# Kernel tuning notes

Measured on AMD Instinct MI355X. Metric: run time of the kernel, lower is better.

The kernel has to match this reference:

```python
import jax, jax.numpy as jnp
import numpy as np

NEUMANN_TERMS = 6  # matches neumann_terms=6 in init_kwargs


def cayley_apply(W, x, terms):
    """Apply Cayley-parameterized unitary U = (I - A)^{-1}(I + A), A = skew(W),
    with the inverse approximated by a truncated Neumann series:
    (I - A)^{-1} z ~= sum_{k=0}^{terms-1} A^k z.  x: [N, d] row vectors."""
    A = 0.5 * (W - W.T)            # skew-symmetric [d, d]
    z = x + x @ A.T                # (I + A) x
    acc = z
    s = z
    for _ in range(terms - 1):     # small fixed loop over Neumann terms
        s = s @ A.T                # A^k z
        acc = acc + s
    return acc


def quantum_activation(h, theta):
    """Parametric quantum rotation: rotate each adjacent feature pair by theta.
    Norm-preserving (unitary) nonlinearity in place of ReLU/GELU."""
    a = h[..., 0::2]
    b = h[..., 1::2]
    c = jnp.cos(theta)
    s = jnp.sin(theta)
    ra = a * c - b * s
    rb = a * s + b * c
    return jnp.stack([ra, rb], axis=-1).reshape(h.shape)


def setup_inputs() -> dict:
    key = jax.random.key(0)
    k1, k2, k3 = jax.random.split(key, 3)
    num_tokens, d_model = 16384, 2048
    x = jax.random.normal(k1, (num_tokens, d_model), dtype=jnp.float32)
    # Orthogonal(gain=0.1)-like init: small-norm weights keep the Neumann series convergent
    u1 = 0.1 * jax.random.normal(k2, (d_model, d_model), dtype=jnp.float32) / jnp.sqrt(d_model)
    u1 = u1 * jnp.sqrt(d_model) * 0.0 + 0.1 * jax.random.orthogonal(k2, d_model, dtype=jnp.float32)
    u2 = 0.1 * jax.random.orthogonal(k3, d_model, dtype=jnp.float32)
    theta = jnp.asarray(0.7854, dtype=jnp.float32)  # pi/4 initializer
    return {"x": x, "u1": u1, "u2": u2, "theta": theta}


def reference(x, u1, u2, theta):
    h = cayley_apply(u1, x, NEUMANN_TERMS)
    h = quantum_activation(h, theta)
    out = cayley_apply(u2, h, NEUMANN_TERMS)
    return out
```

## Files before the change

kernel.cpp:

```cpp
#include <hip/hip_runtime.h>
#include <hip/hip_bf16.h>

#define ND 2048

using bf16 = __hip_bfloat16;
using short8 = __attribute__((ext_vector_type(8))) short;
using floatx4 = __attribute__((ext_vector_type(4))) float;

__device__ __forceinline__ void gl2lds16(const short* g, short* l) {
    __builtin_amdgcn_global_load_lds(
        (const __attribute__((address_space(1))) unsigned int*)g,
        (__attribute__((address_space(3))) unsigned int*)l,
        16, 0, 0);
}


__global__ void build_skew(const float* __restrict__ u, bf16* __restrict__ M) {
    __shared__ float t[32][33];
    const int bx = blockIdx.x & (ND / 32 - 1);
    const int by = blockIdx.x / (ND / 32);
    const int tx = threadIdx.x & 31;
    const int ty = threadIdx.x >> 5;
#pragma unroll
    for (int rr = 0; rr < 4; ++rr) {
        const int r = ty * 4 + rr;
        t[tx][r] = u[(size_t)(bx * 32 + r) * ND + by * 32 + tx];
    }
    __syncthreads();
#pragma unroll
    for (int rr = 0; rr < 4; ++rr) {
        const int r = ty * 4 + rr;
        const size_t idx = (size_t)(by * 32 + r) * ND + bx * 32 + tx;
        M[idx] = __float2bfloat16(0.5f * (t[r][tx] - u[idx]));
    }
}

__global__ void build_hoff1(const bf16* __restrict__ M, const bf16* Msq, bf16* Hoff) {
    const size_t idx = (size_t)blockIdx.x * 256 + threadIdx.x;
    const float m = __bfloat162float(M[idx]);
    const float q = __bfloat162float(Msq[idx]);
    Hoff[idx] = __float2bfloat16(2.f * m + q);
}

__global__ void build_hoff(const bf16* M, const bf16* Msq, bf16* Hoff, bf16* HoffT) {
    const size_t idx = (size_t)blockIdx.x * 256 + threadIdx.x;
    const float m = __bfloat162float(M[idx]);
    const float q = __bfloat162float(Msq[idx]);
    Hoff[idx] = __float2bfloat16(2.f * m + q);
    HoffT[idx] = __float2bfloat16(q - 2.f * m);
}

__global__ void convert_f32_bf16(const float* __restrict__ x, bf16* __restrict__ y) {
    const size_t base = ((size_t)blockIdx.x * 256 + threadIdx.x) * 8;
    const float4 f0 = *(const float4*)(x + base);
    const float4 f1 = *(const float4*)(x + base + 4);
    short8 pk;
    pk[0] = __builtin_bit_cast(short, __float2bfloat16(f0.x));
    pk[1] = __builtin_bit_cast(short, __float2bfloat16(f0.y));
    pk[2] = __builtin_bit_cast(short, __float2bfloat16(f0.z));
    pk[3] = __builtin_bit_cast(short, __float2bfloat16(f0.w));
    pk[4] = __builtin_bit_cast(short, __float2bfloat16(f1.x));
    pk[5] = __builtin_bit_cast(short, __float2bfloat16(f1.y));
    pk[6] = __builtin_bit_cast(short, __float2bfloat16(f1.z));
    pk[7] = __builtin_bit_cast(short, __float2bfloat16(f1.w));
    *(short8*)((short*)y + base) = pk;
}

enum { EPI_PLAIN = 0, EPI_NEG = 1, EPI_ADD1 = 2, EPI_P = 3, EPI_P_ROT = 4, EPI_PT = 5 };

template <int EPI, bool OF32>
__device__ __forceinline__ void gemm_core(
    short* aT, short* bT,
    const bf16* __restrict__ A, const bf16* __restrict__ Bt, void* __restrict__ Cp,
    const int Nc, const int K, const int bx, const int by,
    const bf16* __restrict__ add1, const bf16* __restrict__ add2,
    const float* __restrict__ thetaP)
{
    const int tid = threadIdx.x;
    const int lane = tid & 63;
    const int quad = lane >> 4;
    const int l15 = lane & 15;
    const int wv = tid >> 6;
    const int wr = (wv >> 1) << 6;
    const int wc = (wv & 1) << 6;

    const short* Ag = (const short*)A + (size_t)(by << 7) * K;
    const short* Bg = (const short*)Bt + (size_t)(bx << 7) * K;

    floatx4 acc[4][4];
#pragma unroll
    for (int i = 0; i < 4; ++i)
#pragma unroll
        for (int j = 0; j < 4; ++j)
            acc[i][j] = (floatx4){0.f, 0.f, 0.f, 0.f};

    for (int k0 = 0; k0 < K; k0 += 32) {
#pragma unroll
        for (int c = 0; c < 2; ++c) {
            const int ch = (c << 8) + (wv << 6) + lane;
            const int row = ch >> 2;
            const int kp = (ch & 3) << 3;
            const int ldsBase = ((c << 8) + (wv << 6)) << 3;
            gl2lds16(Ag + (size_t)row * K + k0 + kp, aT + ldsBase);
            gl2lds16(Bg + (size_t)row * K + k0 + kp, bT + ldsBase);
        }
        __syncthreads();
        short8 af[4], bfr[4];
#pragma unroll
        for (int mi = 0; mi < 4; ++mi)
            af[mi] = *(const short8*)(aT + ((wr + (mi << 4) + l15) << 5) + (quad << 3));
#pragma unroll
        for (int ni = 0; ni < 4; ++ni)
            bfr[ni] = *(const short8*)(bT + ((wc + (ni << 4) + l15) << 5) + (quad << 3));
#pragma unroll
        for (int mi = 0; mi < 4; ++mi)
#pragma unroll
            for (int ni = 0; ni < 4; ++ni)
                acc[mi][ni] = __builtin_amdgcn_mfma_f32_16x16x32_bf16(af[mi], bfr[ni], acc[mi][ni], 0, 0, 0);
        __syncthreads();
    }

    float ct = 0.f, st = 0.f;
    if (EPI == EPI_P_ROT) {
        const float th = *thetaP;
        ct = cosf(th);
        st = sinf(th);
    }

#pragma unroll
    for (int mi = 0; mi < 4; ++mi) {
#pragma unroll
        for (int ni = 0; ni < 4; ++ni) {
#pragma unroll
            for (int r = 0; r < 4; ++r) {
                const int row = (by << 7) + wr + (mi << 4) + (quad << 2) + r;
                const int col = (bx << 7) + wc + (ni << 4) + l15;
                const size_t idx = (size_t)row * Nc + col;
                float v = acc[mi][ni][r];
                if (EPI == EPI_NEG) v = -v;
                if (EPI == EPI_ADD1) v += __bfloat162float(add1[idx]);
                if (EPI == EPI_P)
                    v += (row == col ? 1.f : 0.f)
                       + __bfloat162float(add1[idx]) + __bfloat162float(add2[idx]);
                if (EPI == EPI_PT)
                    v += (row == col ? 1.f : 0.f)
                       + __bfloat162float(add1[idx])
                       + __bfloat162float(add2[(size_t)col * Nc + row]);
                if (EPI == EPI_P_ROT) {
                    v += (row == col ? 1.f : 0.f)
                       + __bfloat162float(add1[idx]) + __bfloat162float(add2[idx]);
                    const float w = __shfl_xor(v, 1, 64);
                    v = (l15 & 1) ? (st * w + ct * v) : (ct * v - st * w);
                }
                if (OF32) ((float*)Cp)[idx] = v;
                else      ((bf16*)Cp)[idx] = __float2bfloat16(v);
            }
        }
    }
}

template <int EPI, bool OF32>
__launch_bounds__(256, 2) __global__
void gemm_one(const bf16* __restrict__ A, const bf16* __restrict__ Bt,
              void* __restrict__ Cp, const int Nc, const int K,
              const bf16* __restrict__ add1, const bf16* __restrict__ add2,
              const float* __restrict__ thetaP)
{
    __shared__ __attribute__((aligned(16))) short aT[128 * 32];
    __shared__ __attribute__((aligned(16))) short bT[128 * 32];
    const int nblk = Nc >> 7;
    gemm_core<EPI, OF32>(aT, bT, A, Bt, Cp, Nc, K, blockIdx.x % nblk, blockIdx.x / nblk,
                         add1, add2, thetaP);
}

template <int EPI0, int EPI1>
__launch_bounds__(256, 2) __global__
void gemm_dual(const bf16* A0, const bf16* B0, bf16* C0, const bf16* a10, const bf16* a20,
               const bf16* A1, const bf16* B1, bf16* C1, const bf16* a11, const bf16* a21,
               const float* thetaP)
{
    __shared__ __attribute__((aligned(16))) short aT[128 * 32];
    __shared__ __attribute__((aligned(16))) short bT[128 * 32];
    const int nblk = ND >> 7;
    const int nsub = nblk * nblk;
    int b = blockIdx.x;
    if (b < nsub) {
        gemm_core<EPI0, false>(aT, bT, A0, B0, (void*)C0, ND, ND, b % nblk, b / nblk, a10, a20, thetaP);
    } else {
        b -= nsub;
        gemm_core<EPI1, false>(aT, bT, A1, B1, (void*)C1, ND, ND, b % nblk, b / nblk, a11, a21, thetaP);
    }
}

template <int EPI, bool AF32, bool OF32>
__launch_bounds__(256, 2) __global__
void gemm_bt(const void* __restrict__ Ap, const bf16* __restrict__ Bt,
             void* __restrict__ Cp, const int Nc, const int K,
             const bf16* __restrict__ add1, const bf16* __restrict__ add2,
             const float* __restrict__ thetaP)
{
    __shared__ __attribute__((aligned(16))) short aT[128 * 32];
    __shared__ __attribute__((aligned(16))) short bT[128 * 32];

    const int nblk = Nc >> 7;
    const int bx = blockIdx.x % nblk;
    const int by = blockIdx.x / nblk;
    const int tid = threadIdx.x;
    const int lane = tid & 63;
    const int quad = lane >> 4;
    const int l15 = lane & 15;
    const int wv = tid >> 6;
    const int wr = (wv >> 1) << 6;
    const int wc = (wv & 1) << 6;

    const short* Ag = (const short*)Ap + (size_t)(by << 7) * K;
    const float* Agf = (const float*)Ap + (size_t)(by << 7) * K;
    const short* Bg = (const short*)Bt + (size_t)(bx << 7) * K;

    floatx4 acc[4][4];
#pragma unroll
    for (int i = 0; i < 4; ++i)
#pragma unroll
        for (int j = 0; j < 4; ++j)
            acc[i][j] = (floatx4){0.f, 0.f, 0.f, 0.f};

    for (int k0 = 0; k0 < K; k0 += 32) {
#pragma unroll
        for (int c = 0; c < 2; ++c) {
            const int ch = tid + (c << 8);
            const int row = ch >> 2;
            const int kp = (ch & 3) << 3;
            if (AF32) {
                const float4 f0 = *(const float4*)(Agf + (size_t)row * K + k0 + kp);
                const float4 f1 = *(const float4*)(Agf + (size_t)row * K + k0 + kp + 4);
                short8 pk;
                pk[0] = __builtin_bit_cast(short, __float2bfloat16(f0.x));
                pk[1] = __builtin_bit_cast(short, __float2bfloat16(f0.y));
                pk[2] = __builtin_bit_cast(short, __float2bfloat16(f0.z));
                pk[3] = __builtin_bit_cast(short, __float2bfloat16(f0.w));
                pk[4] = __builtin_bit_cast(short, __float2bfloat16(f1.x));
                pk[5] = __builtin_bit_cast(short, __float2bfloat16(f1.y));
                pk[6] = __builtin_bit_cast(short, __float2bfloat16(f1.z));
                pk[7] = __builtin_bit_cast(short, __float2bfloat16(f1.w));
                *(short8*)(aT + (row << 5) + kp) = pk;
            } else {
                *(int4*)(aT + (row << 5) + kp) = *(const int4*)(Ag + (size_t)row * K + k0 + kp);
            }
            *(int4*)(bT + (row << 5) + kp) = *(const int4*)(Bg + (size_t)row * K + k0 + kp);
        }
        __syncthreads();
        short8 af[4], bfr[4];
#pragma unroll
        for (int mi = 0; mi < 4; ++mi)
            af[mi] = *(const short8*)(aT + ((wr + (mi << 4) + l15) << 5) + (quad << 3));
#pragma unroll
        for (int ni = 0; ni < 4; ++ni)
            bfr[ni] = *(const short8*)(bT + ((wc + (ni << 4) + l15) << 5) + (quad << 3));
#pragma unroll
        for (int mi = 0; mi < 4; ++mi)
#pragma unroll
            for (int ni = 0; ni < 4; ++ni)
                acc[mi][ni] = __builtin_amdgcn_mfma_f32_16x16x32_bf16(af[mi], bfr[ni], acc[mi][ni], 0, 0, 0);
        __syncthreads();
    }

    float ct = 0.f, st = 0.f;
    if (EPI == EPI_P_ROT) {
        const float th = *thetaP;
        ct = cosf(th);
        st = sinf(th);
    }

#pragma unroll
    for (int mi = 0; mi < 4; ++mi) {
#pragma unroll
        for (int ni = 0; ni < 4; ++ni) {
#pragma unroll
            for (int r = 0; r < 4; ++r) {
                const int row = (by << 7) + wr + (mi << 4) + (quad << 2) + r;
                const int col = (bx << 7) + wc + (ni << 4) + l15;
                const size_t idx = (size_t)row * Nc + col;
                float v = acc[mi][ni][r];
                if (EPI == EPI_NEG) v = -v;
                if (EPI == EPI_ADD1) v += __bfloat162float(add1[idx]);
                if (EPI == EPI_P || EPI == EPI_P_ROT)
                    v += (row == col ? 1.f : 0.f)
                       + __bfloat162float(add1[idx]) + __bfloat162float(add2[idx]);
                if (EPI == EPI_P_ROT) {
                    const float w = __shfl_xor(v, 1, 64);
                    v = (l15 & 1) ? (st * w + ct * v) : (ct * v - st * w);
                }
                if (OF32) ((float*)Cp)[idx] = v;
                else      ((bf16*)Cp)[idx] = __float2bfloat16(v);
            }
        }
    }
}


extern "C" void kernel_launch(void* const* d_in, const int* in_sizes, int n_in,
                              void* d_out, int out_size, void* d_ws, size_t ws_size,
                              hipStream_t stream)
{
    const float* x = (const float*)d_in[0];
    const float* u1 = (const float*)d_in[1];
    const float* u2 = (const float*)d_in[2];
    const float* th = (const float*)d_in[3];
    float* out = (float*)d_out;
    const int tokens = in_sizes[0] / ND;

    const size_t MAT = (size_t)ND * ND;
    const size_t XBE = (size_t)tokens * ND;

    const dim3 blk(256);
    const int gSkew = (ND / 32) * (ND / 32);
    const int gElem = (int)(MAT / 256);
    const int gSm = (ND / 128) * (ND / 128);
    const int gBig = (tokens / 128) * (ND / 128);

    if (ws_size >= (6 * MAT + XBE) * sizeof(bf16)) {
        bf16* base = (bf16*)d_ws;
        bf16* b0 = base;
        bf16* b1 = base + MAT;
        bf16* b2 = base + 2 * MAT;
        bf16* b3 = base + 3 * MAT;
        bf16* b4 = base + 4 * MAT;
        bf16* b5 = base + 5 * MAT;
        bf16* xb = base + 6 * MAT;

        convert_f32_bf16<<<(int)(XBE / 2048), blk, 0, stream>>>(x, xb);
        build_skew<<<gSkew, blk, 0, stream>>>(u2, b0);
        build_skew<<<gSkew, blk, 0, stream>>>(u1, b1);
        gemm_dual<EPI_NEG, EPI_NEG><<<2 * gSm, blk, 0, stream>>>(
            b0, b0, b2, nullptr, nullptr,  b1, b1, b3, nullptr, nullptr, nullptr);
        gemm_dual<EPI_ADD1, EPI_ADD1><<<2 * gSm, blk, 0, stream>>>(
            b2, b2, b4, b2, nullptr,  b3, b3, b5, b3, nullptr, nullptr);
        build_hoff1<<<gElem, blk, 0, stream>>>(b0, b2, b2);
        build_hoff1<<<gElem, blk, 0, stream>>>(b1, b3, b3);
        gemm_dual<EPI_PT, EPI_P_ROT><<<2 * gSm, blk, 0, stream>>>(
            b4, b2, b0, b4, b2,  b3, b5, b1, b5, b3, th);
        gemm_one<EPI_PLAIN, false><<<gSm, blk, 0, stream>>>(b0, b1, b2, ND, ND, nullptr, nullptr, nullptr);
        gemm_one<EPI_PLAIN, true><<<gBig, blk, 0, stream>>>(xb, b2, out, ND, ND, nullptr, nullptr, nullptr);
    } else {
        bf16* A = (bf16*)d_ws;
        bf16* B = A + MAT;
        bf16* Cb = B + MAT;
        bf16* D = Cb + MAT;
        bf16* E = D + MAT;

        build_skew<<<gSkew, blk, 0, stream>>>(u2, A);
        gemm_bt<EPI_NEG, false, false><<<gSm, blk, 0, stream>>>(A, A, B, ND, ND, nullptr, nullptr, nullptr);
        gemm_bt<EPI_ADD1, false, false><<<gSm, blk, 0, stream>>>(B, B, Cb, ND, ND, B, nullptr, nullptr);
        build_hoff<<<gElem, blk, 0, stream>>>(A, B, D, E);
        gemm_bt<EPI_P, false, false><<<gSm, blk, 0, stream>>>(Cb, D, A, ND, ND, Cb, E, nullptr);

        build_skew<<<gSkew, blk, 0, stream>>>(u1, B);
        gemm_bt<EPI_NEG, false, false><<<gSm, blk, 0, stream>>>(B, B, Cb, ND, ND, nullptr, nullptr, nullptr);
        gemm_bt<EPI_ADD1, false, false><<<gSm, blk, 0, stream>>>(Cb, Cb, D, ND, ND, Cb, nullptr, nullptr);
        build_hoff<<<gElem, blk, 0, stream>>>(B, Cb, E, B);
        gemm_bt<EPI_P_ROT, false, false><<<gSm, blk, 0, stream>>>(E, D, Cb, ND, ND, D, E, th);

        gemm_bt<EPI_PLAIN, false, false><<<gSm, blk, 0, stream>>>(A, Cb, D, ND, ND, nullptr, nullptr, nullptr);
        gemm_bt<EPI_PLAIN, true, true><<<gBig, blk, 0, stream>>>(x, D, out, ND, ND, nullptr, nullptr, nullptr);
    }
}
```

Before: 624.6 us.

## Add 256x256-tile 8-wave GEMM with phased LDS pipelining for big token GEMM

Adds a new GEMM kernel for the final token-by-d_model product that uses 256x256 output tiles, 512 threads, 128KB LDS double buffering, and a four-phase schedule interleaving global-to-LDS loads with MFMA groups using barriers and setprio. Larger tiles raise arithmetic intensity and reduce global traffic relative to the 128x128 kernel. It is used only when token count is a multiple of 256, otherwise falling back. Risks include lower occupancy from heavy LDS and register use and fragile waitcnt accounting.

```diff
diff --git a/kernel.cpp b/kernel.cpp
--- a/kernel.cpp
+++ b/kernel.cpp
@@ -192,6 +192,184 @@
     }
 }
 
+
+__device__ __forceinline__ void stage512(short* ldsT, const short* gT, const int K,
+                                         const int kb, const int c0,
+                                         const int wv, const int lane) {
+    const int ch = c0 + (wv << 6) + lane;
+    const int rw = ch >> 3;
+    const int cs = (ch & 7) ^ (rw & 7);
+    gl2lds16(gT + (size_t)rw * K + kb + (cs << 3),
+             ldsT + ((c0 + (wv << 6)) << 3));
+}
+
+__device__ __forceinline__ void phase_mid() {
+    __builtin_amdgcn_sched_barrier(0);
+    __builtin_amdgcn_s_barrier();
+    asm volatile("s_waitcnt lgkmcnt(0)" ::: "memory");
+    __builtin_amdgcn_sched_barrier(0);
+    __builtin_amdgcn_s_setprio(1);
+}
+__device__ __forceinline__ void phase_end() {
+    __builtin_amdgcn_s_setprio(0);
+    __builtin_amdgcn_sched_barrier(0);
+    __builtin_amdgcn_s_barrier();
+}
+
+__device__ __forceinline__ void tile256(
+    short* Ac, short* Bc, short* An,
+    const short* Ag, const short* Bg, const int K, const int nt, const int t,
+    const int wv, const int lane, const int aBase, const int bBase,
+    const int cOff0, const int cOff1, floatx4 (&acc)[8][4])
+{
+    short8 af[4][2], bb[4][2];
+    const int kb1 = (t + 1) << 6;
+    const int kb2 = (t + 2) << 6;
+
+#pragma unroll
+    for (int ml = 0; ml < 4; ++ml) {
+        af[ml][0] = *(const short8*)(Ac + aBase + (ml << 10) + cOff0);
+        af[ml][1] = *(const short8*)(Ac + aBase + (ml << 10) + cOff1);
+    }
+#pragma unroll
+    for (int ni = 0; ni < 2; ++ni) {
+        bb[ni][0] = *(const short8*)(Bc + bBase + (ni << 10) + cOff0);
+        bb[ni][1] = *(const short8*)(Bc + bBase + (ni << 10) + cOff1);
+    }
+    if (t + 1 < nt) { stage512(An, Ag, K, kb1, 512, wv, lane); stage512(An, Ag, K, kb1, 1536, wv, lane); }
+    phase_mid();
+#pragma unroll
+    for (int ml = 0; ml < 4; ++ml)
+#pragma unroll
+        for (int ni = 0; ni < 2; ++ni) {
+            acc[ml][ni] = __builtin_amdgcn_mfma_f32_16x16x32_bf16(af[ml][0], bb[ni][0], acc[ml][ni], 0, 0, 0);
+            acc[ml][ni] = __builtin_amdgcn_mfma_f32_16x16x32_bf16(af[ml][1], bb[ni][1], acc[ml][ni], 0, 0, 0);
+        }
+    phase_end();
+
+#pragma unroll
+    for (int ni = 2; ni < 4; ++ni) {
+        bb[ni][0] = *(const short8*)(Bc + bBase + (ni << 10) + cOff0);
+        bb[ni][1] = *(const short8*)(Bc + bBase + (ni << 10) + cOff1);
+    }
+    if (t + 2 < nt) { stage512(Ac, Ag, K, kb2, 0, wv, lane); stage512(Ac, Ag, K, kb2, 1024, wv, lane); }
+    phase_mid();
+#pragma unroll
+    for (int ml = 0; ml < 4; ++ml)
+#pragma unroll
+        for (int ni = 2; ni < 4; ++ni) {
+            acc[ml][ni] = __builtin_amdgcn_mfma_f32_16x16x32_bf16(af[ml][0], bb[ni][0], acc[ml][ni], 0, 0, 0);
+            acc[ml][ni] = __builtin_amdgcn_mfma_f32_16x16x32_bf16(af[ml][1], bb[ni][1], acc[ml][ni], 0, 0, 0);
+        }
+    phase_end();
+
+#pragma unroll
+    for (int ml = 0; ml < 4; ++ml) {
+        af[ml][0] = *(const short8*)(Ac + aBase + 4096 + (ml << 10) + cOff0);
+        af[ml][1] = *(const short8*)(Ac + aBase + 4096 + (ml << 10) + cOff1);
+    }
+    if (t + 2 < nt) { stage512(Bc, Bg, K, kb2, 0, wv, lane); stage512(Bc, Bg, K, kb2, 512, wv, lane); }
+    phase_mid();
+#pragma unroll
+    for (int ml = 0; ml < 4; ++ml)
+#pragma unroll
+        for (int ni = 0; ni < 2; ++ni) {
+            acc[4 + ml][ni] = __builtin_amdgcn_mfma_f32_16x16x32_bf16(af[ml][0], bb[ni][0], acc[4 + ml][ni], 0, 0, 0);
+            acc[4 + ml][ni] = __builtin_amdgcn_mfma_f32_16x16x32_bf16(af[ml][1], bb[ni][1], acc[4 + ml][ni], 0, 0, 0);
+        }
+    phase_end();
+
+    if (t + 2 < nt) { stage512(Bc, Bg, K, kb2, 1024, wv, lane); stage512(Bc, Bg, K, kb2, 1536, wv, lane); }
+    __builtin_amdgcn_sched_barrier(0);
+    if (t < nt - 2) asm volatile("s_waitcnt vmcnt(6)" ::: "memory");
+    else            asm volatile("s_waitcnt vmcnt(0)" ::: "memory");
+    __builtin_amdgcn_s_barrier();
+    __builtin_amdgcn_sched_barrier(0);
+    __builtin_amdgcn_s_setprio(1);
+#pragma unroll
+    for (int ml = 0; ml < 4; ++ml)
+#pragma unroll
+        for (int ni = 2; ni < 4; ++ni) {
+            acc[4 + ml][ni] = __builtin_amdgcn_mfma_f32_16x16x32_bf16(af[ml][0], bb[ni][0], acc[4 + ml][ni], 0, 0, 0);
+            acc[4 + ml][ni] = __builtin_amdgcn_mfma_f32_16x16x32_bf16(af[ml][1], bb[ni][1], acc[4 + ml][ni], 0, 0, 0);
+        }
+    phase_end();
+}
+
+__launch_bounds__(512, 2) __global__
+void gemm_big256(const bf16* __restrict__ A, const bf16* __restrict__ Bt,
+                 float* __restrict__ C, const int Nc, const int K)
+{
+    __shared__ __attribute__((aligned(16))) short smem[65536];
+    short* A0s = smem;
+    short* A1s = smem + 16384;
+    short* B0s = smem + 32768;
+    short* B1s = smem + 49152;
+
+    const int nblkx = Nc >> 8;
+    const int bx = blockIdx.x % nblkx;
+    const int by = blockIdx.x / nblkx;
+    const int tid = threadIdx.x;
+    const int lane = tid & 63;
+    const int q = lane >> 4;
+    const int l15 = lane & 15;
+    const int wv = tid >> 6;
+    const int wm = wv >> 2;
+    const int wn = wv & 3;
+
+    const short* Ag = (const short*)A + (size_t)(by << 8) * K;
+    const short* Bg = (const short*)Bt + (size_t)(bx << 8) * K;
+
+    const int swz = l15 & 7;
+    const int aBase = ((wm << 7) + l15) << 6;
+    const int bBase = ((wn << 6) + l15) << 6;
+    const int cOff0 = (q ^ swz) << 3;
+    const int cOff1 = ((q + 4) ^ swz) << 3;
+
+    floatx4 acc[8][4];
+#pragma unroll
+    for (int i = 0; i < 8; ++i)
+#pragma unroll
+        for (int j = 0; j < 4; ++j)
+            acc[i][j] = (floatx4){0.f, 0.f, 0.f, 0.f};
+
+    const int nt = K >> 6;
+
+    stage512(A0s, Ag, K, 0, 0,    wv, lane);
+    stage512(A0s, Ag, K, 0, 512,  wv, lane);
+    stage512(A0s, Ag, K, 0, 1024, wv, lane);
+    stage512(A0s, Ag, K, 0, 1536, wv, lane);
+    stage512(B0s, Bg, K, 0, 0,    wv, lane);
+    stage512(B0s, Bg, K, 0, 512,  wv, lane);
+    stage512(B0s, Bg, K, 0, 1024, wv, lane);
+    stage512(B0s, Bg, K, 0, 1536, wv, lane);
+    stage512(A1s, Ag, K, 64, 0,    wv, lane);
+    stage512(A1s, Ag, K, 64, 1024, wv, lane);
+    stage512(B1s, Bg, K, 64, 0,    wv, lane);
+    stage512(B1s, Bg, K, 64, 512,  wv, lane);
+    stage512(B1s, Bg, K, 64, 1024, wv, lane);
+    stage512(B1s, Bg, K, 64, 1536, wv, lane);
+    __builtin_amdgcn_sched_barrier(0);
+    asm volatile("s_waitcnt vmcnt(6)" ::: "memory");
+    __builtin_amdgcn_s_barrier();
+
+    for (int t = 0; t < nt; t += 2) {
+        tile256(A0s, B0s, A1s, Ag, Bg, K, nt, t,     wv, lane, aBase, bBase, cOff0, cOff1, acc);
+        tile256(A1s, B1s, A0s, Ag, Bg, K, nt, t + 1, wv, lane, aBase, bBase, cOff0, cOff1, acc);
+    }
+
+#pragma unroll
+    for (int mi = 0; mi < 8; ++mi)
+#pragma unroll
+        for (int ni = 0; ni < 4; ++ni)
+#pragma unroll
+            for (int r = 0; r < 4; ++r) {
+                const int row = (by << 8) + (wm << 7) + (mi << 4) + (q << 2) + r;
+                const int col = (bx << 8) + (wn << 6) + (ni << 4) + l15;
+                C[(size_t)row * Nc + col] = acc[mi][ni][r];
+            }
+}
+
 template <int EPI, bool AF32, bool OF32>
 __launch_bounds__(256, 2) __global__
 void gemm_bt(const void* __restrict__ Ap, const bf16* __restrict__ Bt,
@@ -340,7 +518,12 @@
         gemm_dual<EPI_PT, EPI_P_ROT><<<2 * gSm, blk, 0, stream>>>(
             b4, b2, b0, b4, b2,  b3, b5, b1, b5, b3, th);
         gemm_one<EPI_PLAIN, false><<<gSm, blk, 0, stream>>>(b0, b1, b2, ND, ND, nullptr, nullptr, nullptr);
-        gemm_one<EPI_PLAIN, true><<<gBig, blk, 0, stream>>>(xb, b2, out, ND, ND, nullptr, nullptr, nullptr);
+        if ((tokens & 255) == 0) {
+            const int gBig256 = (tokens >> 8) * (ND >> 8);
+            gemm_big256<<<gBig256, dim3(512), 0, stream>>>(xb, b2, out, ND, ND);
+        } else {
+            gemm_one<EPI_PLAIN, true><<<gBig, blk, 0, stream>>>(xb, b2, out, ND, ND, nullptr, nullptr, nullptr);
+        }
     } else {
         bf16* A = (bf16*)d_ws;
         bf16* B = A + MAT;
```

After: 598.6 us. -4.2%, faster.
